# Kernel tuning notes

Measured on AMD Instinct MI355X. Metric: run time of the kernel, lower is better.

The kernel has to match this reference:

```python
import jax, jax.numpy as jnp
import numpy as np

N_NODES = 100000
N_EDGES = 1600000
N_GRAPHS = 512


def gcn_conv(x, src, dst, W, b, num_nodes):
    """PyG GCNConv: add self-loops, sym-normalize, aggregate, add bias."""
    xw = x @ W  # [N, out]
    # degree over destination nodes, +1 for the implicit self-loop
    deg = jax.ops.segment_sum(jnp.ones(src.shape[0], xw.dtype), dst,
                              num_segments=num_nodes) + 1.0
    dinv = jax.lax.rsqrt(deg)  # deg >= 1, safe
    norm = dinv[src] * dinv[dst]  # [E]
    agg = jax.ops.segment_sum(xw[src] * norm[:, None], dst,
                              num_segments=num_nodes)
    # self-loop contribution: dinv[i]^2 * xw[i]
    agg = agg + xw * (dinv * dinv)[:, None]
    return agg + b


def global_mean_pool(x, batch, num_graphs):
    sums = jax.ops.segment_sum(x, batch, num_segments=num_graphs)
    cnts = jax.ops.segment_sum(jnp.ones(x.shape[0], x.dtype), batch,
                               num_segments=num_graphs)
    return sums / jnp.maximum(cnts, 1.0)[:, None]


def setup_inputs() -> dict:
    key = jax.random.key(0)
    ks = jax.random.split(key, 9)
    x = jax.random.normal(ks[0], (N_NODES, 3), dtype=jnp.float32)
    edge_index = jax.random.randint(ks[1], (2, N_EDGES), 0, N_NODES, dtype=jnp.int64)
    batch = jnp.sort(jax.random.randint(ks[2], (N_NODES,), 0, N_GRAPHS, dtype=jnp.int64))
    W1 = jax.random.normal(ks[3], (3, 32), dtype=jnp.float32) * 0.5
    b1 = jax.random.normal(ks[4], (32,), dtype=jnp.float32) * 0.1
    W2 = jax.random.normal(ks[5], (32, 32), dtype=jnp.float32) * 0.2
    b2 = jax.random.normal(ks[6], (32,), dtype=jnp.float32) * 0.1
    Wl = jax.random.normal(ks[7], (32, 2), dtype=jnp.float32) * 0.2
    bl = jax.random.normal(ks[8], (2,), dtype=jnp.float32) * 0.1
    return {"x": x, "edge_index": edge_index, "batch": batch,
            "W1": W1, "b1": b1, "W2": W2, "b2": b2, "Wl": Wl, "bl": bl}


def reference(x, edge_index, batch, W1, b1, W2, b2, Wl, bl):
    src, dst = edge_index[0], edge_index[1]
    h = jax.nn.relu(gcn_conv(x, src, dst, W1, b1, N_NODES))
    h = jax.nn.relu(gcn_conv(h, src, dst, W2, b2, N_NODES))
    g = global_mean_pool(h, batch, N_GRAPHS)  # [G, 32]
    return g @ Wl + bl  # [G, 2]
```

## Files before the change

### kernel.cpp

```cpp
#include <hip/hip_runtime.h>
#include <hip/hip_fp16.h>

#define NN 100000
#define NE 1600000
#define NG 512
#define F  32

#define BSH    8
#define BNODES 256
#define NB     ((NN + BNODES - 1) / BNODES)
#define CAP    5120
#define PCHUNK 4096
#define EPT    8
#define NWGP   ((NE + PCHUNK - 1) / PCHUNK)

__global__ void k_partition(const int* __restrict__ src, const int* __restrict__ dst,
                            int* __restrict__ cursor, int* __restrict__ part) {
    __shared__ int   s_cnt[NB];
    __shared__ int   s_lstart[NB];
    __shared__ int   s_base[NB];
    __shared__ int   wsum[8];
    __shared__ int   lsort[PCHUNK];
    __shared__ short lbkt[PCHUNK];
    int tid = threadIdx.x;
    for (int i = tid; i < NB; i += 512) s_cnt[i] = 0;
    __syncthreads();
    int e0 = blockIdx.x * PCHUNK;
    int rem = NE - e0;
    int pk[EPT]; short bk[EPT];
    int m = 0;
    if (rem >= PCHUNK) {
#pragma unroll
        for (int h = 0; h < 2; ++h) {
            int e = e0 + h * 2048 + tid * 4;
            int4 s4 = *(const int4*)(src + e);
            int4 d4 = *(const int4*)(dst + e);
            int ss[4] = {s4.x, s4.y, s4.z, s4.w};
            int dd[4] = {d4.x, d4.y, d4.z, d4.w};
#pragma unroll
            for (int u = 0; u < 4; ++u) {
                pk[m] = (ss[u] << 8) | (dd[u] & (BNODES - 1));
                bk[m] = (short)(dd[u] >> BSH);
                atomicAdd(&s_cnt[bk[m]], 1);
                ++m;
            }
        }
    } else {
#pragma unroll
        for (int k = 0; k < EPT; ++k) {
            int e = e0 + tid + k * 512;
            if (e < NE) {
                int d = dst[e];
                pk[m] = (src[e] << 8) | (d & (BNODES - 1));
                bk[m] = (short)(d >> BSH);
                atomicAdd(&s_cnt[bk[m]], 1);
                ++m;
            }
        }
    }
    __syncthreads();
    int cv = (tid < NB) ? s_cnt[tid] : 0;
    int v = cv;
#pragma unroll
    for (int o = 1; o < 64; o <<= 1) {
        int t = __shfl_up(v, o, 64);
        if ((tid & 63) >= o) v += t;
    }
    if ((tid & 63) == 63) wsum[tid >> 6] = v;
    __syncthreads();
    int add = 0;
    for (int w = 0; w < (tid >> 6); ++w) add += wsum[w];
    int excl = v + add - cv;
    if (tid < NB) {
        s_lstart[tid] = excl;
        if (cv) s_base[tid] = tid * CAP + atomicAdd(&cursor[tid], cv);
        s_cnt[tid] = 0;
    }
    __syncthreads();
    for (int k = 0; k < m; ++k) {
        int b = bk[k];
        int r = s_lstart[b] + atomicAdd(&s_cnt[b], 1);
        lsort[r] = pk[k];
        lbkt[r]  = (short)b;
    }
    __syncthreads();
    int cnt = min(rem, PCHUNK);
    for (int i = tid; i < cnt; i += 512) {
        int b = lbkt[i];
        part[s_base[b] + (i - s_lstart[b])] = lsort[i];
    }
}

__global__ void k_build(const int* __restrict__ part, const int* __restrict__ cursor,
                        const float* __restrict__ x,
                        int* __restrict__ rowpack, float* __restrict__ dinv,
                        float4* __restrict__ xd, int* __restrict__ csr) {
    __shared__ __align__(16) int lcsr[CAP];
    __shared__ int hcnt[BNODES];
    __shared__ int off[BNODES];
    __shared__ int wsum[4];
    int b = blockIdx.x, tid = threadIdx.x;
    int node0 = b << BSH;
    int s0 = b * CAP;
    int ec = cursor[b];
    hcnt[tid] = 0;
    __syncthreads();
    int ctail = ec & ~3;
    for (int i = tid * 4; i < ctail; i += 1024) {
        int4 p = *(const int4*)(part + s0 + i);
        atomicAdd(&hcnt[p.x & (BNODES - 1)], 1);
        atomicAdd(&hcnt[p.y & (BNODES - 1)], 1);
        atomicAdd(&hcnt[p.z & (BNODES - 1)], 1);
        atomicAdd(&hcnt[p.w & (BNODES - 1)], 1);
    }
    if (tid < ec - ctail) atomicAdd(&hcnt[part[s0 + ctail + tid] & (BNODES - 1)], 1);
    __syncthreads();
    int c = hcnt[tid];
    int v = c;
#pragma unroll
    for (int o = 1; o < 64; o <<= 1) {
        int t = __shfl_up(v, o, 64);
        if ((tid & 63) >= o) v += t;
    }
    if ((tid & 63) == 63) wsum[tid >> 6] = v;
    __syncthreads();
    int add = 0;
    for (int w = 0; w < (tid >> 6); ++w) add += wsum[w];
    int excl = v + add - c;
    int n = node0 + tid;
    if (n < NN) {
        rowpack[n] = ((s0 + excl) << 10) | c;
        float d = rsqrtf((float)c + 1.0f);
        dinv[n] = d;
        xd[n] = make_float4(d * x[n * 3 + 0], d * x[n * 3 + 1], d * x[n * 3 + 2], d);
    }
    off[tid] = excl;
    __syncthreads();
    for (int i = tid * 4; i < ctail; i += 1024) {
        int4 p = *(const int4*)(part + s0 + i);
        { int pos = atomicAdd(&off[p.x & (BNODES - 1)], 1); lcsr[pos] = p.x >> 8; }
        { int pos = atomicAdd(&off[p.y & (BNODES - 1)], 1); lcsr[pos] = p.y >> 8; }
        { int pos = atomicAdd(&off[p.z & (BNODES - 1)], 1); lcsr[pos] = p.z >> 8; }
        { int pos = atomicAdd(&off[p.w & (BNODES - 1)], 1); lcsr[pos] = p.w >> 8; }
    }
    if (tid < ec - ctail) {
        int p = part[s0 + ctail + tid];
        int pos = atomicAdd(&off[p & (BNODES - 1)], 1);
        lcsr[pos] = p >> 8;
    }
    __syncthreads();
    for (int i = tid * 4; i < ctail; i += 1024)
        *(int4*)(csr + s0 + i) = *(const int4*)(lcsr + i);
    if (tid < ec - ctail) csr[s0 + ctail + tid] = lcsr[ctail + tid];
}

#define L1NPB 32
__global__ void k_l1(const int* __restrict__ rowpack, const int* __restrict__ csr,
                     const float4* __restrict__ xd,
                     const float* __restrict__ W1, const float* __restrict__ b1,
                     __half2* __restrict__ g1) {
    __shared__ float W1s[3 * F];
    __shared__ float b1s[F];
    int tid = threadIdx.x;
    if (tid < 3 * F) W1s[tid] = W1[tid];
    if (tid < F) b1s[tid] = b1[tid];
    __syncthreads();
    int nl = tid >> 3, l8 = tid & 7;
    int n = blockIdx.x * L1NPB + nl;
    if (n >= NN) return;
    int pack = rowpack[n];
    int beg = pack >> 10, deg = pack & 1023;
    float ax = 0.0f, ay = 0.0f, az = 0.0f;
    for (int e = beg + l8; e < beg + deg; e += 8) {
        float4 v = xd[csr[e]];
        ax += v.x; ay += v.y; az += v.z;
    }
#pragma unroll
    for (int o = 1; o < 8; o <<= 1) {
        ax += __shfl_xor(ax, o, 8);
        ay += __shfl_xor(ay, o, 8);
        az += __shfl_xor(az, o, 8);
    }
    float4 sf = xd[n];
    float dn = sf.w;
    float cx = dn * (ax + sf.x), cy = dn * (ay + sf.y), cz = dn * (az + sf.z);
    __half2 tmp[2];
#pragma unroll
    for (int t = 0; t < 2; ++t) {
        int f0 = l8 * 4 + 2 * t, f1 = f0 + 1;
        float v0 = cx * W1s[f0] + cy * W1s[F + f0] + cz * W1s[2 * F + f0] + b1s[f0];
        float v1 = cx * W1s[f1] + cy * W1s[F + f1] + cz * W1s[2 * F + f1] + b1s[f1];
        tmp[t] = __floats2half2_rn(dn * fmaxf(v0, 0.0f), dn * fmaxf(v1, 0.0f));
    }
    *(uint2*)(g1 + (size_t)n * 16 + l8 * 2) = *(const uint2*)tmp;
}

#define SEGCAP 1024
__global__ void k_gather2p(const int* __restrict__ rowpack, const int* __restrict__ csr,
                           const __half2* __restrict__ g1, const float* __restrict__ dinv,
                           const int* __restrict__ batch,
                           const float* __restrict__ W2, const float* __restrict__ b2,
                           float* __restrict__ gsum) {
    __shared__ __align__(16) float W2s[F * F];
    __shared__ __align__(16) float b2s[F];
    __shared__ float ts[16][F];
    __shared__ float hs[16][F];
    __shared__ int bat[16];
    __shared__ int lc[SEGCAP];
    int tid = threadIdx.x;
    int nb = blockIdx.x * 16;
    ((float4*)W2s)[tid] = ((const float4*)W2)[tid];
    if (tid < F / 4) ((float4*)b2s)[tid] = ((const float4*)b2)[tid];
    if (tid < 16) bat[tid] = batch[nb + tid];
    int rp0  = rowpack[nb];
    int rp15 = rowpack[nb + 15];
    int beg0 = rp0 >> 10;
    int seg  = (rp15 >> 10) + (rp15 & 1023) - beg0;
    bool useLds = (seg <= SEGCAP);
    if (useLds) {
        for (int i = tid; i < seg; i += 256) lc[i] = csr[beg0 + i];
    }
    __syncthreads();
    int nl = tid >> 4, j = tid & 15;
    int n = nb + nl;
    {
        int pack = rowpack[n];
        int deg = pack & 1023;
        float ax = 0.0f, ay = 0.0f;
        if (useLds) {
            int e = (pack >> 10) - beg0;
            int end = e + deg;
            for (; e + 7 < end; e += 8) {
                int s0 = lc[e],     s1 = lc[e + 1], s2 = lc[e + 2], s3 = lc[e + 3];
                int s4 = lc[e + 4], s5 = lc[e + 5], s6 = lc[e + 6], s7 = lc[e + 7];
                float2 v0 = __half22float2(g1[s0 * 16 + j]);
                float2 v1 = __half22float2(g1[s1 * 16 + j]);
                float2 v2 = __half22float2(g1[s2 * 16 + j]);
                float2 v3 = __half22float2(g1[s3 * 16 + j]);
                float2 v4 = __half22float2(g1[s4 * 16 + j]);
                float2 v5 = __half22float2(g1[s5 * 16 + j]);
                float2 v6 = __half22float2(g1[s6 * 16 + j]);
                float2 v7 = __half22float2(g1[s7 * 16 + j]);
                ax += ((v0.x + v1.x) + (v2.x + v3.x)) + ((v4.x + v5.x) + (v6.x + v7.x));
                ay += ((v0.y + v1.y) + (v2.y + v3.y)) + ((v4.y + v5.y) + (v6.y + v7.y));
            }
            for (; e + 3 < end; e += 4) {
                int s0 = lc[e], s1 = lc[e + 1], s2 = lc[e + 2], s3 = lc[e + 3];
                float2 v0 = __half22float2(g1[s0 * 16 + j]);
                float2 v1 = __half22float2(g1[s1 * 16 + j]);
                float2 v2 = __half22float2(g1[s2 * 16 + j]);
                float2 v3 = __half22float2(g1[s3 * 16 + j]);
                ax += (v0.x + v1.x) + (v2.x + v3.x);
                ay += (v0.y + v1.y) + (v2.y + v3.y);
            }
            for (; e < end; ++e) {
                float2 v = __half22float2(g1[lc[e] * 16 + j]);
                ax += v.x; ay += v.y;
            }
        } else {
            int e = pack >> 10;
            int end = e + deg;
            for (; e < end; ++e) {
                float2 v = __half22float2(g1[csr[e] * 16 + j]);
                ax += v.x; ay += v.y;
            }
        }
        float dn = dinv[n];
        float2 sf = __half22float2(g1[n * 16 + j]);
        ts[nl][2 * j]     = dn * (ax + sf.x);
        ts[nl][2 * j + 1] = dn * (ay + sf.y);
    }
    __syncthreads();
    {
        int f = tid & 31;
        int nn0 = tid >> 5;
#pragma unroll
        for (int pass = 0; pass < 2; ++pass) {
            int nn = nn0 + pass * 8;
            float acc = b2s[f];
#pragma unroll
            for (int k = 0; k < F; ++k) acc += ts[nn][k] * W2s[k * F + f];
            hs[nn][f] = fmaxf(acc, 0.0f);
        }
    }
    __syncthreads();
    if (tid < F) {
        int g0 = bat[0], gmax = bat[15];
        for (int g = g0; g <= gmax; ++g) {
            float s = 0.0f;
#pragma unroll
            for (int i = 0; i < 16; ++i) if (bat[i] == g) s += hs[i][tid];
            atomicAdd(&gsum[g * F + tid], s);
        }
    }
}

__global__ void k_head(const float* __restrict__ gsum, const int* __restrict__ batch,
                       const float* __restrict__ Wl, const float* __restrict__ bl,
                       float* __restrict__ out) {
    int g = blockIdx.x * blockDim.x + threadIdx.x;
    if (g >= NG) return;
    int lo = 0, hi = NN;
    while (lo < hi) { int m = (lo + hi) >> 1; if (batch[m] < g) lo = m + 1; else hi = m; }
    int s = lo;
    lo = 0; hi = NN;
    while (lo < hi) { int m = (lo + hi) >> 1; if (batch[m] < g + 1) lo = m + 1; else hi = m; }
    float inv = 1.0f / fmaxf((float)(lo - s), 1.0f);
    float a0 = 0.0f, a1 = 0.0f;
#pragma unroll
    for (int k = 0; k < F; ++k) {
        float m = gsum[g * F + k] * inv;
        a0 += m * Wl[k * 2 + 0];
        a1 += m * Wl[k * 2 + 1];
    }
    out[g * 2 + 0] = a0 + bl[0];
    out[g * 2 + 1] = a1 + bl[1];
}

extern "C" void kernel_launch(void* const* d_in, const int* in_sizes, int n_in,
                              void* d_out, int out_size, void* d_ws, size_t ws_size,
                              hipStream_t stream) {
    const float* x     = (const float*)d_in[0];
    const int*   eidx  = (const int*)d_in[1];
    const int*   batch = (const int*)d_in[2];
    const float* W1    = (const float*)d_in[3];
    const float* b1    = (const float*)d_in[4];
    const float* W2    = (const float*)d_in[5];
    const float* b2    = (const float*)d_in[6];
    const float* Wl    = (const float*)d_in[7];
    const float* bl    = (const float*)d_in[8];
    float*       out   = (float*)d_out;

    const int* src = eidx;
    const int* dst = eidx + NE;

    char* base = (char*)d_ws;
    size_t off = 0;
    auto alloc = [&](size_t bytes) {
        void* p = base + off;
        off = (off + bytes + 127) & ~(size_t)127;
        return p;
    };
    int*     cursor  = (int*)alloc(NB * sizeof(int) + (size_t)NG * F * sizeof(float));
    float*   gsum    = (float*)(cursor + NB);
    int*     rowpack = (int*)alloc(NN * sizeof(int));
    int*     part    = (int*)alloc((size_t)NB * CAP * sizeof(int));
    int*     csr     = (int*)alloc((size_t)NB * CAP * sizeof(int));
    float*   dinv    = (float*)alloc(NN * sizeof(float));
    float4*  xd      = (float4*)alloc(NN * sizeof(float4));
    __half2* g1      = (__half2*)alloc((size_t)NN * 16 * sizeof(__half2));

    const int B = 256;
    const int gL1  = (NN + L1NPB - 1) / L1NPB;
    const int gG16 = NN / 16;

    hipMemsetAsync(cursor, 0, NB * sizeof(int) + (size_t)NG * F * sizeof(float), stream);

    k_partition<<<NWGP, 512, 0, stream>>>(src, dst, cursor, part);
    k_build    <<<NB,   B,   0, stream>>>(part, cursor, x, rowpack, dinv, xd, csr);

    k_l1<<<gL1, B, 0, stream>>>(rowpack, csr, xd, W1, b1, g1);

    k_gather2p<<<gG16, B, 0, stream>>>(rowpack, csr, g1, dinv, batch, W2, b2, gsum);

    k_head<<<(NG + B - 1) / B, B, 0, stream>>>(gsum, batch, Wl, bl, out);
}
```

Measured before the change: 153.9 us.

## Gather layer-2 rows with 16-byte loads, 4 threads per node, 64 nodes per block

Rework the layer-2 gather so each node is handled by 4 lanes, each loading a uint4 (8 halves) per neighbour instead of 16 lanes loading a half2. Each block now covers 64 nodes instead of 16, which spreads the W2 load and the pooling atomics over more nodes and cuts the number of blocks. It also adds tail handling for a partial last block. The cost is fewer threads per node, which lowers memory-level parallelism per row and lengthens the serial neighbour loop. The larger per-block segment may also exceed the LDS cap more often and fall back to reading the edge list from global memory.

Result: slower. 165.7 us (+7.7%).

```diff
diff --git a/kernel.cpp b/kernel.cpp
--- a/kernel.cpp
+++ b/kernel.cpp
@@ -195,7 +195,8 @@
     *(uint2*)(g1 + (size_t)n * 16 + l8 * 2) = *(const uint2*)tmp;
 }
 
-#define SEGCAP 1024
+#define G2NPB  64
+#define SEGCAP 1280
 __global__ void k_gather2p(const int* __restrict__ rowpack, const int* __restrict__ csr,
                            const __half2* __restrict__ g1, const float* __restrict__ dinv,
                            const int* __restrict__ batch,
@@ -203,79 +204,87 @@
                            float* __restrict__ gsum) {
     __shared__ __align__(16) float W2s[F * F];
     __shared__ __align__(16) float b2s[F];
-    __shared__ float ts[16][F];
-    __shared__ float hs[16][F];
-    __shared__ int bat[16];
+    __shared__ float ts[G2NPB][F];
+    __shared__ float hs[G2NPB][F];
+    __shared__ int bat[G2NPB];
     __shared__ int lc[SEGCAP];
     int tid = threadIdx.x;
-    int nb = blockIdx.x * 16;
+    int nb = blockIdx.x * G2NPB;
+    int vmax = min(G2NPB, NN - nb);
     ((float4*)W2s)[tid] = ((const float4*)W2)[tid];
     if (tid < F / 4) ((float4*)b2s)[tid] = ((const float4*)b2)[tid];
-    if (tid < 16) bat[tid] = batch[nb + tid];
-    int rp0  = rowpack[nb];
-    int rp15 = rowpack[nb + 15];
+    if (tid < vmax) bat[tid] = batch[nb + tid];
+    int rp0 = rowpack[nb];
+    int rpL = rowpack[nb + vmax - 1];
     int beg0 = rp0 >> 10;
-    int seg  = (rp15 >> 10) + (rp15 & 1023) - beg0;
+    int seg  = (rpL >> 10) + (rpL & 1023) - beg0;
     bool useLds = (seg <= SEGCAP);
     if (useLds) {
         for (int i = tid; i < seg; i += 256) lc[i] = csr[beg0 + i];
     }
     __syncthreads();
-    int nl = tid >> 4, j = tid & 15;
+    int nl = tid >> 2, l4 = tid & 3;
     int n = nb + nl;
-    {
+    if (n < NN) {
         int pack = rowpack[n];
         int deg = pack & 1023;
-        float ax = 0.0f, ay = 0.0f;
+        float a0 = 0, a1 = 0, a2 = 0, a3 = 0, a4 = 0, a5 = 0, a6 = 0, a7 = 0;
+        const uint4* g4 = (const uint4*)g1;
         if (useLds) {
             int e = (pack >> 10) - beg0;
             int end = e + deg;
-            for (; e + 7 < end; e += 8) {
-                int s0 = lc[e],     s1 = lc[e + 1], s2 = lc[e + 2], s3 = lc[e + 3];
-                int s4 = lc[e + 4], s5 = lc[e + 5], s6 = lc[e + 6], s7 = lc[e + 7];
-                float2 v0 = __half22float2(g1[s0 * 16 + j]);
-                float2 v1 = __half22float2(g1[s1 * 16 + j]);
-                float2 v2 = __half22float2(g1[s2 * 16 + j]);
-                float2 v3 = __half22float2(g1[s3 * 16 + j]);
-                float2 v4 = __half22float2(g1[s4 * 16 + j]);
-                float2 v5 = __half22float2(g1[s5 * 16 + j]);
-                float2 v6 = __half22float2(g1[s6 * 16 + j]);
-                float2 v7 = __half22float2(g1[s7 * 16 + j]);
-                ax += ((v0.x + v1.x) + (v2.x + v3.x)) + ((v4.x + v5.x) + (v6.x + v7.x));
-                ay += ((v0.y + v1.y) + (v2.y + v3.y)) + ((v4.y + v5.y) + (v6.y + v7.y));
-            }
-            for (; e + 3 < end; e += 4) {
-                int s0 = lc[e], s1 = lc[e + 1], s2 = lc[e + 2], s3 = lc[e + 3];
-                float2 v0 = __half22float2(g1[s0 * 16 + j]);
-                float2 v1 = __half22float2(g1[s1 * 16 + j]);
-                float2 v2 = __half22float2(g1[s2 * 16 + j]);
-                float2 v3 = __half22float2(g1[s3 * 16 + j]);
-                ax += (v0.x + v1.x) + (v2.x + v3.x);
-                ay += (v0.y + v1.y) + (v2.y + v3.y);
-            }
-            for (; e < end; ++e) {
-                float2 v = __half22float2(g1[lc[e] * 16 + j]);
-                ax += v.x; ay += v.y;
+            for (; e + 1 < end; e += 2) {
+                uint4 u = g4[lc[e] * 4 + l4];
+                uint4 w = g4[lc[e + 1] * 4 + l4];
+                float2 p;
+                p = __half22float2(*(const __half2*)&u.x); a0 += p.x; a1 += p.y;
+                p = __half22float2(*(const __half2*)&u.y); a2 += p.x; a3 += p.y;
+                p = __half22float2(*(const __half2*)&u.z); a4 += p.x; a5 += p.y;
+                p = __half22float2(*(const __half2*)&u.w); a6 += p.x; a7 += p.y;
+                p = __half22float2(*(const __half2*)&w.x); a0 += p.x; a1 += p.y;
+                p = __half22float2(*(const __half2*)&w.y); a2 += p.x; a3 += p.y;
+                p = __half22float2(*(const __half2*)&w.z); a4 += p.x; a5 += p.y;
+                p = __half22float2(*(const __half2*)&w.w); a6 += p.x; a7 += p.y;
+            }
+            if (e < end) {
+                uint4 u = g4[lc[e] * 4 + l4];
+                float2 p;
+                p = __half22float2(*(const __half2*)&u.x); a0 += p.x; a1 += p.y;
+                p = __half22float2(*(const __half2*)&u.y); a2 += p.x; a3 += p.y;
+                p = __half22float2(*(const __half2*)&u.z); a4 += p.x; a5 += p.y;
+                p = __half22float2(*(const __half2*)&u.w); a6 += p.x; a7 += p.y;
             }
         } else {
             int e = pack >> 10;
             int end = e + deg;
             for (; e < end; ++e) {
-                float2 v = __half22float2(g1[csr[e] * 16 + j]);
-                ax += v.x; ay += v.y;
+                uint4 u = g4[csr[e] * 4 + l4];
+                float2 p;
+                p = __half22float2(*(const __half2*)&u.x); a0 += p.x; a1 += p.y;
+                p = __half22float2(*(const __half2*)&u.y); a2 += p.x; a3 += p.y;
+                p = __half22float2(*(const __half2*)&u.z); a4 += p.x; a5 += p.y;
+                p = __half22float2(*(const __half2*)&u.w); a6 += p.x; a7 += p.y;
             }
         }
         float dn = dinv[n];
-        float2 sf = __half22float2(g1[n * 16 + j]);
-        ts[nl][2 * j]     = dn * (ax + sf.x);
-        ts[nl][2 * j + 1] = dn * (ay + sf.y);
+        uint4 su = g4[(size_t)n * 4 + l4];
+        float2 p;
+        float* tr = &ts[nl][l4 * 8];
+        p = __half22float2(*(const __half2*)&su.x); tr[0] = dn * (a0 + p.x); tr[1] = dn * (a1 + p.y);
+        p = __half22float2(*(const __half2*)&su.y); tr[2] = dn * (a2 + p.x); tr[3] = dn * (a3 + p.y);
+        p = __half22float2(*(const __half2*)&su.z); tr[4] = dn * (a4 + p.x); tr[5] = dn * (a5 + p.y);
+        p = __half22float2(*(const __half2*)&su.w); tr[6] = dn * (a6 + p.x); tr[7] = dn * (a7 + p.y);
+    } else {
+        float* tr = &ts[nl][l4 * 8];
+#pragma unroll
+        for (int k = 0; k < 8; ++k) tr[k] = 0.0f;
     }
     __syncthreads();
     {
         int f = tid & 31;
         int nn0 = tid >> 5;
 #pragma unroll
-        for (int pass = 0; pass < 2; ++pass) {
+        for (int pass = 0; pass < 8; ++pass) {
             int nn = nn0 + pass * 8;
             float acc = b2s[f];
 #pragma unroll
@@ -285,11 +294,10 @@
     }
     __syncthreads();
     if (tid < F) {
-        int g0 = bat[0], gmax = bat[15];
+        int g0 = bat[0], gmax = bat[vmax - 1];
         for (int g = g0; g <= gmax; ++g) {
             float s = 0.0f;
-#pragma unroll
-            for (int i = 0; i < 16; ++i) if (bat[i] == g) s += hs[i][tid];
+            for (int i = 0; i < vmax; ++i) if (bat[i] == g) s += hs[i][tid];
             atomicAdd(&gsum[g * F + tid], s);
         }
     }
@@ -351,8 +359,8 @@
     __half2* g1      = (__half2*)alloc((size_t)NN * 16 * sizeof(__half2));
 
     const int B = 256;
-    const int gL1  = (NN + L1NPB - 1) / L1NPB;
-    const int gG16 = NN / 16;
+    const int gL1 = (NN + L1NPB - 1) / L1NPB;
+    const int gG2 = (NN + G2NPB - 1) / G2NPB;
 
     hipMemsetAsync(cursor, 0, NB * sizeof(int) + (size_t)NG * F * sizeof(float), stream);
 
@@ -361,7 +369,7 @@
 
     k_l1<<<gL1, B, 0, stream>>>(rowpack, csr, xd, W1, b1, g1);
 
-    k_gather2p<<<gG16, B, 0, stream>>>(rowpack, csr, g1, dinv, batch, W2, b2, gsum);
+    k_gather2p<<<gG2, B, 0, stream>>>(rowpack, csr, g1, dinv, batch, W2, b2, gsum);
 
     k_head<<<(NG + B - 1) / B, B, 0, stream>>>(gsum, batch, Wl, bl, out);
 }
```

## Fuse all GCN stages into one persistent kernel with grid-wide barriers

Applied to the files above, without the earlier changes.

Replaces the five separate kernel launches with a single persistent kernel of 512 blocks that loops over the work of each stage and separates stages with an atomic-counter grid barrier. The aim is to remove launch gaps and tail effects between the short stages. Block sizes and per-iteration node counts also change (512 threads, 64 nodes per layer-1 tile, 32 nodes per layer-2 tile, smaller LDS segment cap). The spin barrier relies on all 512 blocks being co-resident; if they are not, the kernel deadlocks. The barrier also serialises stages and can leave CUs idle during load imbalance.

Measured after the change: 390.0 us. 153% more time.

```diff
diff --git a/kernel.cpp b/kernel.cpp
--- a/kernel.cpp
+++ b/kernel.cpp
@@ -11,310 +11,330 @@
 #define NB     ((NN + BNODES - 1) / BNODES)
 #define CAP    5120
 #define PCHUNK 4096
+#define NWGP   ((NE + PCHUNK - 1) / PCHUNK)
 #define EPT    8
-#define NWGP   ((NE + PCHUNK - 1) / PCHUNK)
-
-__global__ void k_partition(const int* __restrict__ src, const int* __restrict__ dst,
-                            int* __restrict__ cursor, int* __restrict__ part) {
-    __shared__ int   s_cnt[NB];
-    __shared__ int   s_lstart[NB];
-    __shared__ int   s_base[NB];
-    __shared__ int   wsum[8];
-    __shared__ int   lsort[PCHUNK];
-    __shared__ short lbkt[PCHUNK];
-    int tid = threadIdx.x;
-    for (int i = tid; i < NB; i += 512) s_cnt[i] = 0;
+
+#define GRID   512
+#define BT     512
+#define L1V    ((NN + 63) / 64)
+#define G2V    (NN / 32)
+#define SEGCAP 768
+
+struct Params {
+    const int* src; const int* dst;
+    const float* x; const int* batch;
+    const float* W1; const float* b1;
+    const float* W2; const float* b2;
+    const float* Wl; const float* bl;
+    int* bar; int* cursor; float* gsum;
+    int* rowpack; int* part; int* csr;
+    float* dinv; float4* xd; __half2* g1;
+    float* out;
+};
+
+union __align__(16) SharedU {
+    struct { int lsort[PCHUNK]; short lbkt[PCHUNK];
+             int s_cnt[NB]; int s_lstart[NB]; int s_base[NB]; int wsum[8]; } p1;
+    struct { __align__(16) int lcsr[CAP]; int hcnt[BNODES]; int off[BNODES]; int wsum[4]; } p2;
+    struct { float W1s[3 * F]; float b1s[F]; } p3;
+    struct { __align__(16) float W2s[F * F]; float b2s[F];
+             float ts[32][F]; float hs[32][F]; int bat[32]; int lc[SEGCAP]; } p4;
+};
+
+__device__ __forceinline__ void gbar(int* ctr, int target) {
     __syncthreads();
-    int e0 = blockIdx.x * PCHUNK;
-    int rem = NE - e0;
-    int pk[EPT]; short bk[EPT];
-    int m = 0;
-    if (rem >= PCHUNK) {
-#pragma unroll
-        for (int h = 0; h < 2; ++h) {
-            int e = e0 + h * 2048 + tid * 4;
-            int4 s4 = *(const int4*)(src + e);
-            int4 d4 = *(const int4*)(dst + e);
-            int ss[4] = {s4.x, s4.y, s4.z, s4.w};
-            int dd[4] = {d4.x, d4.y, d4.z, d4.w};
-#pragma unroll
-            for (int u = 0; u < 4; ++u) {
-                pk[m] = (ss[u] << 8) | (dd[u] & (BNODES - 1));
-                bk[m] = (short)(dd[u] >> BSH);
-                atomicAdd(&s_cnt[bk[m]], 1);
-                ++m;
-            }
-        }
-    } else {
-#pragma unroll
-        for (int k = 0; k < EPT; ++k) {
-            int e = e0 + tid + k * 512;
-            if (e < NE) {
-                int d = dst[e];
-                pk[m] = (src[e] << 8) | (d & (BNODES - 1));
-                bk[m] = (short)(d >> BSH);
-                atomicAdd(&s_cnt[bk[m]], 1);
-                ++m;
-            }
-        }
+    if (threadIdx.x == 0) {
+        __threadfence();
+        atomicAdd(ctr, 1);
+        while (atomicAdd(ctr, 0) < target) { }
+        __threadfence();
     }
     __syncthreads();
-    int cv = (tid < NB) ? s_cnt[tid] : 0;
-    int v = cv;
-#pragma unroll
-    for (int o = 1; o < 64; o <<= 1) {
-        int t = __shfl_up(v, o, 64);
-        if ((tid & 63) >= o) v += t;
-    }
-    if ((tid & 63) == 63) wsum[tid >> 6] = v;
-    __syncthreads();
-    int add = 0;
-    for (int w = 0; w < (tid >> 6); ++w) add += wsum[w];
-    int excl = v + add - cv;
-    if (tid < NB) {
-        s_lstart[tid] = excl;
-        if (cv) s_base[tid] = tid * CAP + atomicAdd(&cursor[tid], cv);
-        s_cnt[tid] = 0;
-    }
-    __syncthreads();
-    for (int k = 0; k < m; ++k) {
-        int b = bk[k];
-        int r = s_lstart[b] + atomicAdd(&s_cnt[b], 1);
-        lsort[r] = pk[k];
-        lbkt[r]  = (short)b;
-    }
-    __syncthreads();
-    int cnt = min(rem, PCHUNK);
-    for (int i = tid; i < cnt; i += 512) {
-        int b = lbkt[i];
-        part[s_base[b] + (i - s_lstart[b])] = lsort[i];
-    }
 }
 
-__global__ void k_build(const int* __restrict__ part, const int* __restrict__ cursor,
-                        const float* __restrict__ x,
-                        int* __restrict__ rowpack, float* __restrict__ dinv,
-                        float4* __restrict__ xd, int* __restrict__ csr) {
-    __shared__ __align__(16) int lcsr[CAP];
-    __shared__ int hcnt[BNODES];
-    __shared__ int off[BNODES];
-    __shared__ int wsum[4];
-    int b = blockIdx.x, tid = threadIdx.x;
-    int node0 = b << BSH;
-    int s0 = b * CAP;
-    int ec = cursor[b];
-    hcnt[tid] = 0;
-    __syncthreads();
-    int ctail = ec & ~3;
-    for (int i = tid * 4; i < ctail; i += 1024) {
-        int4 p = *(const int4*)(part + s0 + i);
-        atomicAdd(&hcnt[p.x & (BNODES - 1)], 1);
-        atomicAdd(&hcnt[p.y & (BNODES - 1)], 1);
-        atomicAdd(&hcnt[p.z & (BNODES - 1)], 1);
-        atomicAdd(&hcnt[p.w & (BNODES - 1)], 1);
-    }
-    if (tid < ec - ctail) atomicAdd(&hcnt[part[s0 + ctail + tid] & (BNODES - 1)], 1);
-    __syncthreads();
-    int c = hcnt[tid];
-    int v = c;
-#pragma unroll
-    for (int o = 1; o < 64; o <<= 1) {
-        int t = __shfl_up(v, o, 64);
-        if ((tid & 63) >= o) v += t;
-    }
-    if ((tid & 63) == 63) wsum[tid >> 6] = v;
-    __syncthreads();
-    int add = 0;
-    for (int w = 0; w < (tid >> 6); ++w) add += wsum[w];
-    int excl = v + add - c;
-    int n = node0 + tid;
-    if (n < NN) {
-        rowpack[n] = ((s0 + excl) << 10) | c;
-        float d = rsqrtf((float)c + 1.0f);
-        dinv[n] = d;
-        xd[n] = make_float4(d * x[n * 3 + 0], d * x[n * 3 + 1], d * x[n * 3 + 2], d);
-    }
-    off[tid] = excl;
-    __syncthreads();
-    for (int i = tid * 4; i < ctail; i += 1024) {
-        int4 p = *(const int4*)(part + s0 + i);
-        { int pos = atomicAdd(&off[p.x & (BNODES - 1)], 1); lcsr[pos] = p.x >> 8; }
-        { int pos = atomicAdd(&off[p.y & (BNODES - 1)], 1); lcsr[pos] = p.y >> 8; }
-        { int pos = atomicAdd(&off[p.z & (BNODES - 1)], 1); lcsr[pos] = p.z >> 8; }
-        { int pos = atomicAdd(&off[p.w & (BNODES - 1)], 1); lcsr[pos] = p.w >> 8; }
-    }
-    if (tid < ec - ctail) {
-        int p = part[s0 + ctail + tid];
-        int pos = atomicAdd(&off[p & (BNODES - 1)], 1);
-        lcsr[pos] = p >> 8;
-    }
-    __syncthreads();
-    for (int i = tid * 4; i < ctail; i += 1024)
-        *(int4*)(csr + s0 + i) = *(const int4*)(lcsr + i);
-    if (tid < ec - ctail) csr[s0 + ctail + tid] = lcsr[ctail + tid];
-}
-
-#define L1NPB 32
-__global__ void k_l1(const int* __restrict__ rowpack, const int* __restrict__ csr,
-                     const float4* __restrict__ xd,
-                     const float* __restrict__ W1, const float* __restrict__ b1,
-                     __half2* __restrict__ g1) {
-    __shared__ float W1s[3 * F];
-    __shared__ float b1s[F];
-    int tid = threadIdx.x;
-    if (tid < 3 * F) W1s[tid] = W1[tid];
-    if (tid < F) b1s[tid] = b1[tid];
-    __syncthreads();
-    int nl = tid >> 3, l8 = tid & 7;
-    int n = blockIdx.x * L1NPB + nl;
-    if (n >= NN) return;
-    int pack = rowpack[n];
-    int beg = pack >> 10, deg = pack & 1023;
-    float ax = 0.0f, ay = 0.0f, az = 0.0f;
-    for (int e = beg + l8; e < beg + deg; e += 8) {
-        float4 v = xd[csr[e]];
-        ax += v.x; ay += v.y; az += v.z;
-    }
-#pragma unroll
-    for (int o = 1; o < 8; o <<= 1) {
-        ax += __shfl_xor(ax, o, 8);
-        ay += __shfl_xor(ay, o, 8);
-        az += __shfl_xor(az, o, 8);
-    }
-    float4 sf = xd[n];
-    float dn = sf.w;
-    float cx = dn * (ax + sf.x), cy = dn * (ay + sf.y), cz = dn * (az + sf.z);
-    __half2 tmp[2];
-#pragma unroll
-    for (int t = 0; t < 2; ++t) {
-        int f0 = l8 * 4 + 2 * t, f1 = f0 + 1;
-        float v0 = cx * W1s[f0] + cy * W1s[F + f0] + cz * W1s[2 * F + f0] + b1s[f0];
-        float v1 = cx * W1s[f1] + cy * W1s[F + f1] + cz * W1s[2 * F + f1] + b1s[f1];
-        tmp[t] = __floats2half2_rn(dn * fmaxf(v0, 0.0f), dn * fmaxf(v1, 0.0f));
-    }
-    *(uint2*)(g1 + (size_t)n * 16 + l8 * 2) = *(const uint2*)tmp;
-}
-
-#define SEGCAP 1024
-__global__ void k_gather2p(const int* __restrict__ rowpack, const int* __restrict__ csr,
-                           const __half2* __restrict__ g1, const float* __restrict__ dinv,
-                           const int* __restrict__ batch,
-                           const float* __restrict__ W2, const float* __restrict__ b2,
-                           float* __restrict__ gsum) {
-    __shared__ __align__(16) float W2s[F * F];
-    __shared__ __align__(16) float b2s[F];
-    __shared__ float ts[16][F];
-    __shared__ float hs[16][F];
-    __shared__ int bat[16];
-    __shared__ int lc[SEGCAP];
-    int tid = threadIdx.x;
-    int nb = blockIdx.x * 16;
-    ((float4*)W2s)[tid] = ((const float4*)W2)[tid];
-    if (tid < F / 4) ((float4*)b2s)[tid] = ((const float4*)b2)[tid];
-    if (tid < 16) bat[tid] = batch[nb + tid];
-    int rp0  = rowpack[nb];
-    int rp15 = rowpack[nb + 15];
-    int beg0 = rp0 >> 10;
-    int seg  = (rp15 >> 10) + (rp15 & 1023) - beg0;
-    bool useLds = (seg <= SEGCAP);
-    if (useLds) {
-        for (int i = tid; i < seg; i += 256) lc[i] = csr[beg0 + i];
-    }
-    __syncthreads();
-    int nl = tid >> 4, j = tid & 15;
-    int n = nb + nl;
-    {
-        int pack = rowpack[n];
-        int deg = pack & 1023;
-        float ax = 0.0f, ay = 0.0f;
-        if (useLds) {
-            int e = (pack >> 10) - beg0;
-            int end = e + deg;
-            for (; e + 7 < end; e += 8) {
-                int s0 = lc[e],     s1 = lc[e + 1], s2 = lc[e + 2], s3 = lc[e + 3];
-                int s4 = lc[e + 4], s5 = lc[e + 5], s6 = lc[e + 6], s7 = lc[e + 7];
-                float2 v0 = __half22float2(g1[s0 * 16 + j]);
-                float2 v1 = __half22float2(g1[s1 * 16 + j]);
-                float2 v2 = __half22float2(g1[s2 * 16 + j]);
-                float2 v3 = __half22float2(g1[s3 * 16 + j]);
-                float2 v4 = __half22float2(g1[s4 * 16 + j]);
-                float2 v5 = __half22float2(g1[s5 * 16 + j]);
-                float2 v6 = __half22float2(g1[s6 * 16 + j]);
-                float2 v7 = __half22float2(g1[s7 * 16 + j]);
-                ax += ((v0.x + v1.x) + (v2.x + v3.x)) + ((v4.x + v5.x) + (v6.x + v7.x));
-                ay += ((v0.y + v1.y) + (v2.y + v3.y)) + ((v4.y + v5.y) + (v6.y + v7.y));
-            }
-            for (; e + 3 < end; e += 4) {
-                int s0 = lc[e], s1 = lc[e + 1], s2 = lc[e + 2], s3 = lc[e + 3];
-                float2 v0 = __half22float2(g1[s0 * 16 + j]);
-                float2 v1 = __half22float2(g1[s1 * 16 + j]);
-                float2 v2 = __half22float2(g1[s2 * 16 + j]);
-                float2 v3 = __half22float2(g1[s3 * 16 + j]);
-                ax += (v0.x + v1.x) + (v2.x + v3.x);
-                ay += (v0.y + v1.y) + (v2.y + v3.y);
-            }
-            for (; e < end; ++e) {
-                float2 v = __half22float2(g1[lc[e] * 16 + j]);
-                ax += v.x; ay += v.y;
+__global__ void __launch_bounds__(BT, 4) k_mega(Params P) {
+    __shared__ SharedU S;
+    const int tid = threadIdx.x;
+    const int bid = blockIdx.x;
+
+    for (int c = bid; c < NWGP; c += GRID) {
+        for (int i = tid; i < NB; i += BT) S.p1.s_cnt[i] = 0;
+        __syncthreads();
+        int e0 = c * PCHUNK;
+        int rem = NE - e0;
+        int pk[EPT]; short bk[EPT];
+        int m = 0;
+        if (rem >= PCHUNK) {
+#pragma unroll
+            for (int h = 0; h < 2; ++h) {
+                int e = e0 + h * 2048 + tid * 4;
+                int4 s4 = *(const int4*)(P.src + e);
+                int4 d4 = *(const int4*)(P.dst + e);
+                int ss[4] = {s4.x, s4.y, s4.z, s4.w};
+                int dd[4] = {d4.x, d4.y, d4.z, d4.w};
+#pragma unroll
+                for (int u = 0; u < 4; ++u) {
+                    pk[m] = (ss[u] << 8) | (dd[u] & (BNODES - 1));
+                    bk[m] = (short)(dd[u] >> BSH);
+                    atomicAdd(&S.p1.s_cnt[bk[m]], 1);
+                    ++m;
+                }
             }
         } else {
-            int e = pack >> 10;
-            int end = e + deg;
-            for (; e < end; ++e) {
-                float2 v = __half22float2(g1[csr[e] * 16 + j]);
-                ax += v.x; ay += v.y;
-            }
-        }
-        float dn = dinv[n];
-        float2 sf = __half22float2(g1[n * 16 + j]);
-        ts[nl][2 * j]     = dn * (ax + sf.x);
-        ts[nl][2 * j + 1] = dn * (ay + sf.y);
-    }
+#pragma unroll
+            for (int k = 0; k < EPT; ++k) {
+                int e = e0 + tid + k * BT;
+                if (e < NE) {
+                    int d = P.dst[e];
+                    pk[m] = (P.src[e] << 8) | (d & (BNODES - 1));
+                    bk[m] = (short)(d >> BSH);
+                    atomicAdd(&S.p1.s_cnt[bk[m]], 1);
+                    ++m;
+                }
+            }
+        }
+        __syncthreads();
+        int cv = (tid < NB) ? S.p1.s_cnt[tid] : 0;
+        int v = cv;
+#pragma unroll
+        for (int o = 1; o < 64; o <<= 1) {
+            int t = __shfl_up(v, o, 64);
+            if ((tid & 63) >= o) v += t;
+        }
+        if ((tid & 63) == 63) S.p1.wsum[tid >> 6] = v;
+        __syncthreads();
+        int add = 0;
+        for (int w = 0; w < (tid >> 6); ++w) add += S.p1.wsum[w];
+        int excl = v + add - cv;
+        if (tid < NB) {
+            S.p1.s_lstart[tid] = excl;
+            if (cv) S.p1.s_base[tid] = tid * CAP + atomicAdd(&P.cursor[tid], cv);
+            S.p1.s_cnt[tid] = 0;
+        }
+        __syncthreads();
+        for (int k = 0; k < m; ++k) {
+            int b = bk[k];
+            int r = S.p1.s_lstart[b] + atomicAdd(&S.p1.s_cnt[b], 1);
+            S.p1.lsort[r] = pk[k];
+            S.p1.lbkt[r]  = (short)b;
+        }
+        __syncthreads();
+        int cnt = min(rem, PCHUNK);
+        for (int i = tid; i < cnt; i += BT) {
+            int b = S.p1.lbkt[i];
+            P.part[S.p1.s_base[b] + (i - S.p1.s_lstart[b])] = S.p1.lsort[i];
+        }
+        __syncthreads();
+    }
+    gbar(P.bar, GRID * 1);
+
+    for (int b = bid; b < NB; b += GRID) {
+        int node0 = b << BSH;
+        int s0 = b * CAP;
+        int ec = P.cursor[b];
+        if (tid < BNODES) S.p2.hcnt[tid] = 0;
+        __syncthreads();
+        int ctail = ec & ~3;
+        for (int i = tid * 4; i < ctail; i += BT * 4) {
+            int4 p = *(const int4*)(P.part + s0 + i);
+            atomicAdd(&S.p2.hcnt[p.x & (BNODES - 1)], 1);
+            atomicAdd(&S.p2.hcnt[p.y & (BNODES - 1)], 1);
+            atomicAdd(&S.p2.hcnt[p.z & (BNODES - 1)], 1);
+            atomicAdd(&S.p2.hcnt[p.w & (BNODES - 1)], 1);
+        }
+        if (tid < ec - ctail) atomicAdd(&S.p2.hcnt[P.part[s0 + ctail + tid] & (BNODES - 1)], 1);
+        __syncthreads();
+        int c = (tid < BNODES) ? S.p2.hcnt[tid] : 0;
+        int v = c;
+#pragma unroll
+        for (int o = 1; o < 64; o <<= 1) {
+            int t = __shfl_up(v, o, 64);
+            if ((tid & 63) >= o) v += t;
+        }
+        if ((tid & 63) == 63 && tid < BNODES) S.p2.wsum[tid >> 6] = v;
+        __syncthreads();
+        int add = 0;
+        if (tid < BNODES) for (int w = 0; w < (tid >> 6); ++w) add += S.p2.wsum[w];
+        int excl = v + add - c;
+        int n = node0 + tid;
+        if (tid < BNODES) {
+            if (n < NN) {
+                P.rowpack[n] = ((s0 + excl) << 10) | c;
+                float d = rsqrtf((float)c + 1.0f);
+                P.dinv[n] = d;
+                P.xd[n] = make_float4(d * P.x[n * 3 + 0], d * P.x[n * 3 + 1],
+                                      d * P.x[n * 3 + 2], d);
+            }
+            S.p2.off[tid] = excl;
+        }
+        __syncthreads();
+        for (int i = tid * 4; i < ctail; i += BT * 4) {
+            int4 p = *(const int4*)(P.part + s0 + i);
+            { int pos = atomicAdd(&S.p2.off[p.x & (BNODES - 1)], 1); S.p2.lcsr[pos] = p.x >> 8; }
+            { int pos = atomicAdd(&S.p2.off[p.y & (BNODES - 1)], 1); S.p2.lcsr[pos] = p.y >> 8; }
+            { int pos = atomicAdd(&S.p2.off[p.z & (BNODES - 1)], 1); S.p2.lcsr[pos] = p.z >> 8; }
+            { int pos = atomicAdd(&S.p2.off[p.w & (BNODES - 1)], 1); S.p2.lcsr[pos] = p.w >> 8; }
+        }
+        if (tid < ec - ctail) {
+            int p = P.part[s0 + ctail + tid];
+            int pos = atomicAdd(&S.p2.off[p & (BNODES - 1)], 1);
+            S.p2.lcsr[pos] = p >> 8;
+        }
+        __syncthreads();
+        for (int i = tid * 4; i < ctail; i += BT * 4)
+            *(int4*)(P.csr + s0 + i) = *(const int4*)(S.p2.lcsr + i);
+        if (tid < ec - ctail) P.csr[s0 + ctail + tid] = S.p2.lcsr[ctail + tid];
+        __syncthreads();
+    }
+    gbar(P.bar, GRID * 2);
+
+    if (tid < 3 * F) S.p3.W1s[tid] = P.W1[tid];
+    if (tid < F)     S.p3.b1s[tid] = P.b1[tid];
     __syncthreads();
     {
-        int f = tid & 31;
-        int nn0 = tid >> 5;
-#pragma unroll
-        for (int pass = 0; pass < 2; ++pass) {
-            int nn = nn0 + pass * 8;
-            float acc = b2s[f];
-#pragma unroll
-            for (int k = 0; k < F; ++k) acc += ts[nn][k] * W2s[k * F + f];
-            hs[nn][f] = fmaxf(acc, 0.0f);
-        }
-    }
-    __syncthreads();
-    if (tid < F) {
-        int g0 = bat[0], gmax = bat[15];
-        for (int g = g0; g <= gmax; ++g) {
-            float s = 0.0f;
-#pragma unroll
-            for (int i = 0; i < 16; ++i) if (bat[i] == g) s += hs[i][tid];
-            atomicAdd(&gsum[g * F + tid], s);
-        }
-    }
-}
-
-__global__ void k_head(const float* __restrict__ gsum, const int* __restrict__ batch,
-                       const float* __restrict__ Wl, const float* __restrict__ bl,
-                       float* __restrict__ out) {
-    int g = blockIdx.x * blockDim.x + threadIdx.x;
-    if (g >= NG) return;
-    int lo = 0, hi = NN;
-    while (lo < hi) { int m = (lo + hi) >> 1; if (batch[m] < g) lo = m + 1; else hi = m; }
-    int s = lo;
-    lo = 0; hi = NN;
-    while (lo < hi) { int m = (lo + hi) >> 1; if (batch[m] < g + 1) lo = m + 1; else hi = m; }
-    float inv = 1.0f / fmaxf((float)(lo - s), 1.0f);
-    float a0 = 0.0f, a1 = 0.0f;
-#pragma unroll
-    for (int k = 0; k < F; ++k) {
-        float m = gsum[g * F + k] * inv;
-        a0 += m * Wl[k * 2 + 0];
-        a1 += m * Wl[k * 2 + 1];
-    }
-    out[g * 2 + 0] = a0 + bl[0];
-    out[g * 2 + 1] = a1 + bl[1];
+        int nl = tid >> 3, l8 = tid & 7;
+        for (int vb = bid; vb < L1V; vb += GRID) {
+            int n = vb * 64 + nl;
+            if (n < NN) {
+                int pack = P.rowpack[n];
+                int beg = pack >> 10, deg = pack & 1023;
+                float ax = 0.0f, ay = 0.0f, az = 0.0f;
+                for (int e = beg + l8; e < beg + deg; e += 8) {
+                    float4 vv = P.xd[P.csr[e]];
+                    ax += vv.x; ay += vv.y; az += vv.z;
+                }
+#pragma unroll
+                for (int o = 1; o < 8; o <<= 1) {
+                    ax += __shfl_xor(ax, o, 8);
+                    ay += __shfl_xor(ay, o, 8);
+                    az += __shfl_xor(az, o, 8);
+                }
+                float4 sf = P.xd[n];
+                float dn = sf.w;
+                float cx = dn * (ax + sf.x), cy = dn * (ay + sf.y), cz = dn * (az + sf.z);
+                __half2 tmp[2];
+#pragma unroll
+                for (int t = 0; t < 2; ++t) {
+                    int f0 = l8 * 4 + 2 * t, f1 = f0 + 1;
+                    float v0 = cx * S.p3.W1s[f0] + cy * S.p3.W1s[F + f0]
+                             + cz * S.p3.W1s[2 * F + f0] + S.p3.b1s[f0];
+                    float v1 = cx * S.p3.W1s[f1] + cy * S.p3.W1s[F + f1]
+                             + cz * S.p3.W1s[2 * F + f1] + S.p3.b1s[f1];
+                    tmp[t] = __floats2half2_rn(dn * fmaxf(v0, 0.0f), dn * fmaxf(v1, 0.0f));
+                }
+                *(uint2*)(P.g1 + (size_t)n * 16 + l8 * 2) = *(const uint2*)tmp;
+            }
+        }
+    }
+    gbar(P.bar, GRID * 3);
+
+    if (tid < 256) ((float4*)S.p4.W2s)[tid] = ((const float4*)P.W2)[tid];
+    if (tid < F / 4) ((float4*)S.p4.b2s)[tid] = ((const float4*)P.b2)[tid];
+    for (int vb = bid; vb < G2V; vb += GRID) {
+        __syncthreads();
+        int nb = vb * 32;
+        if (tid < 32) S.p4.bat[tid] = P.batch[nb + tid];
+        int rp0 = P.rowpack[nb];
+        int rpL = P.rowpack[nb + 31];
+        int beg0 = rp0 >> 10;
+        int seg  = (rpL >> 10) + (rpL & 1023) - beg0;
+        bool useLds = (seg <= SEGCAP);
+        if (useLds) {
+            for (int i = tid; i < seg; i += BT) S.p4.lc[i] = P.csr[beg0 + i];
+        }
+        __syncthreads();
+        int nl = tid >> 4, j = tid & 15;
+        int n = nb + nl;
+        {
+            int pack = P.rowpack[n];
+            int deg = pack & 1023;
+            float ax = 0.0f, ay = 0.0f;
+            if (useLds) {
+                int e = (pack >> 10) - beg0;
+                int end = e + deg;
+                for (; e + 7 < end; e += 8) {
+                    int s0 = S.p4.lc[e],     s1 = S.p4.lc[e + 1], s2 = S.p4.lc[e + 2], s3 = S.p4.lc[e + 3];
+                    int s4 = S.p4.lc[e + 4], s5 = S.p4.lc[e + 5], s6 = S.p4.lc[e + 6], s7 = S.p4.lc[e + 7];
+                    float2 v0 = __half22float2(P.g1[s0 * 16 + j]);
+                    float2 v1 = __half22float2(P.g1[s1 * 16 + j]);
+                    float2 v2 = __half22float2(P.g1[s2 * 16 + j]);
+                    float2 v3 = __half22float2(P.g1[s3 * 16 + j]);
+                    float2 v4 = __half22float2(P.g1[s4 * 16 + j]);
+                    float2 v5 = __half22float2(P.g1[s5 * 16 + j]);
+                    float2 v6 = __half22float2(P.g1[s6 * 16 + j]);
+                    float2 v7 = __half22float2(P.g1[s7 * 16 + j]);
+                    ax += ((v0.x + v1.x) + (v2.x + v3.x)) + ((v4.x + v5.x) + (v6.x + v7.x));
+                    ay += ((v0.y + v1.y) + (v2.y + v3.y)) + ((v4.y + v5.y) + (v6.y + v7.y));
+                }
+                for (; e + 3 < end; e += 4) {
+                    int s0 = S.p4.lc[e], s1 = S.p4.lc[e + 1], s2 = S.p4.lc[e + 2], s3 = S.p4.lc[e + 3];
+                    float2 v0 = __half22float2(P.g1[s0 * 16 + j]);
+                    float2 v1 = __half22float2(P.g1[s1 * 16 + j]);
+                    float2 v2 = __half22float2(P.g1[s2 * 16 + j]);
+                    float2 v3 = __half22float2(P.g1[s3 * 16 + j]);
+                    ax += (v0.x + v1.x) + (v2.x + v3.x);
+                    ay += (v0.y + v1.y) + (v2.y + v3.y);
+                }
+                for (; e < end; ++e) {
+                    float2 v = __half22float2(P.g1[S.p4.lc[e] * 16 + j]);
+                    ax += v.x; ay += v.y;
+                }
+            } else {
+                int e = pack >> 10;
+                int end = e + deg;
+                for (; e < end; ++e) {
+                    float2 v = __half22float2(P.g1[P.csr[e] * 16 + j]);
+                    ax += v.x; ay += v.y;
+                }
+            }
+            float dn = P.dinv[n];
+            float2 sf = __half22float2(P.g1[n * 16 + j]);
+            S.p4.ts[nl][2 * j]     = dn * (ax + sf.x);
+            S.p4.ts[nl][2 * j + 1] = dn * (ay + sf.y);
+        }
+        __syncthreads();
+        {
+            int f = tid & 31;
+            int nn0 = tid >> 5;
+#pragma unroll
+            for (int pass = 0; pass < 2; ++pass) {
+                int nn = nn0 + pass * 16;
+                float acc = S.p4.b2s[f];
+#pragma unroll
+                for (int k = 0; k < F; ++k) acc += S.p4.ts[nn][k] * S.p4.W2s[k * F + f];
+                S.p4.hs[nn][f] = fmaxf(acc, 0.0f);
+            }
+        }
+        __syncthreads();
+        if (tid < F) {
+            int g0 = S.p4.bat[0], gmax = S.p4.bat[31];
+            for (int g = g0; g <= gmax; ++g) {
+                float s = 0.0f;
+                for (int i = 0; i < 32; ++i) if (S.p4.bat[i] == g) s += S.p4.hs[i][tid];
+                atomicAdd(&P.gsum[g * F + tid], s);
+            }
+        }
+    }
+    gbar(P.bar, GRID * 4);
+
+    if (bid == 0) {
+        int g = tid;
+        int lo = 0, hi = NN;
+        while (lo < hi) { int m = (lo + hi) >> 1; if (P.batch[m] < g) lo = m + 1; else hi = m; }
+        int s = lo;
+        lo = 0; hi = NN;
+        while (lo < hi) { int m = (lo + hi) >> 1; if (P.batch[m] < g + 1) lo = m + 1; else hi = m; }
+        float inv = 1.0f / fmaxf((float)(lo - s), 1.0f);
+        float a0 = 0.0f, a1 = 0.0f;
+#pragma unroll
+        for (int k = 0; k < F; ++k) {
+            float m = P.gsum[g * F + k] * inv;
+            a0 += m * P.Wl[k * 2 + 0];
+            a1 += m * P.Wl[k * 2 + 1];
+        }
+        P.out[g * 2 + 0] = a0 + P.bl[0];
+        P.out[g * 2 + 1] = a1 + P.bl[1];
+    }
 }
 
 extern "C" void kernel_launch(void* const* d_in, const int* in_sizes, int n_in,
@@ -341,7 +361,9 @@
         off = (off + bytes + 127) & ~(size_t)127;
         return p;
     };
-    int*     cursor  = (int*)alloc(NB * sizeof(int) + (size_t)NG * F * sizeof(float));
+    size_t zbytes = 32 * sizeof(int) + NB * sizeof(int) + (size_t)NG * F * sizeof(float);
+    int*     barp    = (int*)alloc(zbytes);
+    int*     cursor  = barp + 32;
     float*   gsum    = (float*)(cursor + NB);
     int*     rowpack = (int*)alloc(NN * sizeof(int));
     int*     part    = (int*)alloc((size_t)NB * CAP * sizeof(int));
@@ -350,18 +372,14 @@
     float4*  xd      = (float4*)alloc(NN * sizeof(float4));
     __half2* g1      = (__half2*)alloc((size_t)NN * 16 * sizeof(__half2));
 
-    const int B = 256;
-    const int gL1  = (NN + L1NPB - 1) / L1NPB;
-    const int gG16 = NN / 16;
-
-    hipMemsetAsync(cursor, 0, NB * sizeof(int) + (size_t)NG * F * sizeof(float), stream);
-
-    k_partition<<<NWGP, 512, 0, stream>>>(src, dst, cursor, part);
-    k_build    <<<NB,   B,   0, stream>>>(part, cursor, x, rowpack, dinv, xd, csr);
-
-    k_l1<<<gL1, B, 0, stream>>>(rowpack, csr, xd, W1, b1, g1);
-
-    k_gather2p<<<gG16, B, 0, stream>>>(rowpack, csr, g1, dinv, batch, W2, b2, gsum);
-
-    k_head<<<(NG + B - 1) / B, B, 0, stream>>>(gsum, batch, Wl, bl, out);
+    hipMemsetAsync(barp, 0, zbytes, stream);
+
+    Params Pv;
+    Pv.src = src; Pv.dst = dst; Pv.x = x; Pv.batch = batch;
+    Pv.W1 = W1; Pv.b1 = b1; Pv.W2 = W2; Pv.b2 = b2; Pv.Wl = Wl; Pv.bl = bl;
+    Pv.bar = barp; Pv.cursor = cursor; Pv.gsum = gsum; Pv.rowpack = rowpack;
+    Pv.part = part; Pv.csr = csr; Pv.dinv = dinv; Pv.xd = xd; Pv.g1 = g1;
+    Pv.out = out;
+
+    k_mega<<<dim3(GRID), dim3(BT), 0, stream>>>(Pv);
 }
```
